# Optimization experiments

Hardware: AMD Instinct MI355X
Metric: run time of the kernel (lower is better)

The kernel has to match this reference:

```python
import jax, jax.numpy as jnp
import numpy as np

# constants from init param dict
WEIGHT = 1.0
SIGMA = 0.15          # color bandwidth
SIGMA_XY = 1.0        # spatial bandwidth
SUB_EPS = 0.01        # subtract_eps
NEG_CLASS = 0         # negative_class
NUM_CLASSES = 2
SHIFTS = ((0, 1), (1, 0), (1, 1), (1, -1))


def _shift(x, dy, dx):
    # out[..., h, w] = x[..., h+dy, w+dx]; out-of-range handled via valid mask
    return jnp.roll(x, (-dy, -dx), axis=(-2, -1))


def _valid(H, W, dy, dx, dtype):
    hs = jnp.arange(H)
    ws = jnp.arange(W)
    vh = (hs + dy >= 0) & (hs + dy < H)
    vw = (ws + dx >= 0) & (ws + dx < W)
    return (vh[:, None] & vw[None, :]).astype(dtype)  # [H, W]


def setup_inputs() -> dict:
    key = jax.random.key(0)
    k1, k2, k3 = jax.random.split(key, 3)
    B, C, H, W = 16, NUM_CLASSES, 512, 512
    # soft predictions (probabilities over classes)
    y_pr = jax.nn.softmax(jax.random.normal(k1, (B, C, H, W), dtype=jnp.float32), axis=1)
    y_gt = jnp.zeros((B, H, W), dtype=jnp.int32)  # unused by the loss
    image = jax.random.uniform(k2, (B, 3, H, W), dtype=jnp.float32)
    image_class = jax.random.randint(k3, (B,), 0, 2)
    return {"y_pr": y_pr, "y_gt": y_gt, "image": image, "image_class": image_class}


def reference(y_pr, y_gt, image, image_class):
    B, _, H, W = image.shape
    # semi-supervised selection: only images not labeled as the negative class
    sel = (image_class != NEG_CLASS).astype(y_pr.dtype)  # [B]
    loss = jnp.asarray(0.0, dtype=y_pr.dtype)
    for (dy, dx) in SHIFTS:
        v = _valid(H, W, dy, dx, y_pr.dtype)                       # [H, W]
        img_sh = _shift(image, dy, dx)                             # [B, 3, H, W]
        d2 = jnp.sum((image - img_sh) ** 2, axis=1)                # [B, H, W]
        w_xy = np.exp(-(dy * dy + dx * dx) / (2.0 * SIGMA_XY ** 2))
        mask = (jnp.exp(-d2 / (2.0 * SIGMA ** 2)) * w_xy - SUB_EPS) * v
        for ch in range(1, NUM_CLASSES):
            y = y_pr[:, ch]                                        # [B, H, W]
            pair = (y - _shift(y, dy, dx)) ** 2 * v                # [B, H, W]
            per_img = jnp.sum(mask * pair, axis=(1, 2)) / (H * W)  # [B]
            loss = loss + jnp.sum(sel * per_img) / B
    return WEIGHT * loss / len(SHIFTS)
```

## Files before the change

### kernel.cpp

```cpp
#include <hip/hip_runtime.h>


#define BATCH 16
#define HGT 512
#define WID 512
#define HW (HGT * WID)
#define SEG 8
#define SEGS_PER_ROW (WID / SEG)
#define SEGS_PER_BATCH (HGT * SEGS_PER_ROW)
#define NSEG (BATCH * SEGS_PER_BATCH)
#define NBLOCK (NSEG / 256)

__global__ __launch_bounds__(256) void crf_map(
        const float* __restrict__ y_pr,
        const float* __restrict__ image,
        const int* __restrict__ image_class,
        double* __restrict__ partial) {
    const float inv2s2 = 22.2222222f;
    const float wxy1 = 0.60653066f;
    const float wxy2 = 0.36787944f;

    const int b = blockIdx.x >> 7;
    double local = 0.0;

    if (image_class[b] != 0) {
        const int idx = blockIdx.x * 256 + threadIdx.x;
        const int seg = idx & (SEGS_PER_BATCH - 1);
        const int h = seg >> 6;
        const int w0 = (seg & 63) * SEG;
        const int hw = h * WID + w0;
        const bool hn = (h + 1 < HGT);
        const bool left = (w0 > 0);
        const bool right = (w0 + SEG < WID);

        const float* __restrict__ yb = y_pr + (size_t)b * 2 * HW + HW;
        const float* __restrict__ ib = image + (size_t)b * 3 * HW;

        float d2r[8], d2d[8], d2dr[8], d2dl[8];
        #pragma unroll
        for (int j = 0; j < 8; j++) { d2r[j] = 0.f; d2d[j] = 0.f; d2dr[j] = 0.f; d2dl[j] = 0.f; }

        #pragma unroll
        for (int c = 0; c < 3; c++) {
            const float* __restrict__ p = ib + c * HW + hw;
            float cur[9], nxt[10];
            {
                float4 a0 = *(const float4*)(p);
                float4 a1 = *(const float4*)(p + 4);
                cur[0] = a0.x; cur[1] = a0.y; cur[2] = a0.z; cur[3] = a0.w;
                cur[4] = a1.x; cur[5] = a1.y; cur[6] = a1.z; cur[7] = a1.w;
                cur[8] = right ? p[8] : 0.f;
            }
            if (hn) {
                float4 b0 = *(const float4*)(p + WID);
                float4 b1 = *(const float4*)(p + WID + 4);
                nxt[0] = left ? p[WID - 1] : 0.f;
                nxt[1] = b0.x; nxt[2] = b0.y; nxt[3] = b0.z; nxt[4] = b0.w;
                nxt[5] = b1.x; nxt[6] = b1.y; nxt[7] = b1.z; nxt[8] = b1.w;
                nxt[9] = right ? p[WID + 8] : 0.f;
            } else {
                #pragma unroll
                for (int k = 0; k < 10; k++) nxt[k] = 0.f;
            }
            #pragma unroll
            for (int j = 0; j < 8; j++) {
                float dr  = cur[j] - cur[j + 1];  d2r[j]  += dr  * dr;
                float dd  = cur[j] - nxt[j + 1];  d2d[j]  += dd  * dd;
                float ddr = cur[j] - nxt[j + 2];  d2dr[j] += ddr * ddr;
                float ddl = cur[j] - nxt[j];      d2dl[j] += ddl * ddl;
            }
        }

        float yc[9], yn[10];
        {
            const float* __restrict__ p = yb + hw;
            float4 a0 = *(const float4*)(p);
            float4 a1 = *(const float4*)(p + 4);
            yc[0] = a0.x; yc[1] = a0.y; yc[2] = a0.z; yc[3] = a0.w;
            yc[4] = a1.x; yc[5] = a1.y; yc[6] = a1.z; yc[7] = a1.w;
            yc[8] = right ? p[8] : 0.f;
            if (hn) {
                float4 b0 = *(const float4*)(p + WID);
                float4 b1 = *(const float4*)(p + WID + 4);
                yn[0] = left ? p[WID - 1] : 0.f;
                yn[1] = b0.x; yn[2] = b0.y; yn[3] = b0.z; yn[4] = b0.w;
                yn[5] = b1.x; yn[6] = b1.y; yn[7] = b1.z; yn[8] = b1.w;
                yn[9] = right ? p[WID + 8] : 0.f;
            } else {
                #pragma unroll
                for (int k = 0; k < 10; k++) yn[k] = 0.f;
            }
        }

        float s = 0.f;
        #pragma unroll
        for (int j = 0; j < 8; j++) {
            if (j < 7 || right) {
                float dy = yc[j] - yc[j + 1];
                float m = expf(-d2r[j] * inv2s2) * wxy1 - 0.01f;
                s += m * dy * dy;
            }
            if (hn) {
                {
                    float dy = yc[j] - yn[j + 1];
                    float m = expf(-d2d[j] * inv2s2) * wxy1 - 0.01f;
                    s += m * dy * dy;
                }
                if (j < 7 || right) {
                    float dy = yc[j] - yn[j + 2];
                    float m = expf(-d2dr[j] * inv2s2) * wxy2 - 0.01f;
                    s += m * dy * dy;
                }
                if (j > 0 || left) {
                    float dy = yc[j] - yn[j];
                    float m = expf(-d2dl[j] * inv2s2) * wxy2 - 0.01f;
                    s += m * dy * dy;
                }
            }
        }
        local = (double)s;
    }

    for (int off = 32; off > 0; off >>= 1)
        local += __shfl_down(local, off);

    __shared__ double sdata[4];
    const int lane = threadIdx.x & 63;
    const int wv = threadIdx.x >> 6;
    if (lane == 0) sdata[wv] = local;
    __syncthreads();
    if (threadIdx.x == 0)
        partial[blockIdx.x] = sdata[0] + sdata[1] + sdata[2] + sdata[3];
}

__global__ __launch_bounds__(256) void crf_reduce(
        const double* __restrict__ partial, float* __restrict__ out) {
    double s = 0.0;
    for (int i = threadIdx.x; i < NBLOCK; i += 256)
        s += partial[i];
    for (int off = 32; off > 0; off >>= 1)
        s += __shfl_down(s, off);
    __shared__ double sdata[4];
    const int lane = threadIdx.x & 63;
    const int wv = threadIdx.x >> 6;
    if (lane == 0) sdata[wv] = s;
    __syncthreads();
    if (threadIdx.x == 0) {
        double t = sdata[0] + sdata[1] + sdata[2] + sdata[3];
        out[0] = (float)(t * (1.0 / ((double)HW * BATCH * 4)));
    }
}

extern "C" void kernel_launch(void* const* d_in, const int* in_sizes, int n_in,
                              void* d_out, int out_size, void* d_ws, size_t ws_size,
                              hipStream_t stream) {
    const float* y_pr = (const float*)d_in[0];
    const float* image = (const float*)d_in[2];
    const int* image_class = (const int*)d_in[3];
    float* out = (float*)d_out;
    double* partial = (double*)d_ws;

    crf_map<<<NBLOCK, 256, 0, stream>>>(y_pr, image, image_class, partial);
    crf_reduce<<<1, 256, 0, stream>>>(partial, out);
}
```

Baseline: 117.3 us.

## Process two rows per thread to reuse middle row loads, use fast exp

Each thread now handles an 8-pixel segment in two consecutive rows, so the middle row's image and prediction values serve both as the lower neighbour of the first row and as the current row of the second. This cuts redundant global and cache loads from roughly two rows per output row to about one and a half, and halves the grid to 1024 blocks. It also switches expf to __expf for cheaper exponentials. The cost is higher register pressure from doubled accumulators and possibly lower occupancy.

```diff
diff --git a/kernel.cpp b/kernel.cpp
--- a/kernel.cpp
+++ b/kernel.cpp
@@ -6,10 +6,7 @@
 #define WID 512
 #define HW (HGT * WID)
 #define SEG 8
-#define SEGS_PER_ROW (WID / SEG)
-#define SEGS_PER_BATCH (HGT * SEGS_PER_ROW)
-#define NSEG (BATCH * SEGS_PER_BATCH)
-#define NBLOCK (NSEG / 256)
+#define NBLOCK 1024
 
 __global__ __launch_bounds__(256) void crf_map(
         const float* __restrict__ y_pr,
@@ -20,72 +17,98 @@
     const float wxy1 = 0.60653066f;
     const float wxy2 = 0.36787944f;
 
-    const int b = blockIdx.x >> 7;
+    const int b = blockIdx.x >> 6;
     double local = 0.0;
 
     if (image_class[b] != 0) {
-        const int idx = blockIdx.x * 256 + threadIdx.x;
-        const int seg = idx & (SEGS_PER_BATCH - 1);
-        const int h = seg >> 6;
-        const int w0 = (seg & 63) * SEG;
+        const int tid = blockIdx.x * 256 + threadIdx.x;
+        const int q = tid & 16383;
+        const int rp = q >> 6;
+        const int w0 = (q & 63) * SEG;
+        const int h = rp * 2;
         const int hw = h * WID + w0;
-        const bool hn = (h + 1 < HGT);
         const bool left = (w0 > 0);
         const bool right = (w0 + SEG < WID);
+        const bool hnB = (rp < 255);
 
         const float* __restrict__ yb = y_pr + (size_t)b * 2 * HW + HW;
         const float* __restrict__ ib = image + (size_t)b * 3 * HW;
 
-        float d2r[8], d2d[8], d2dr[8], d2dl[8];
+        float Ar[8], Ad[8], Adr[8], Adl[8];
+        float Br[8], Bd[8], Bdr[8], Bdl[8];
         #pragma unroll
-        for (int j = 0; j < 8; j++) { d2r[j] = 0.f; d2d[j] = 0.f; d2dr[j] = 0.f; d2dl[j] = 0.f; }
+        for (int j = 0; j < 8; j++) {
+            Ar[j]=0.f; Ad[j]=0.f; Adr[j]=0.f; Adl[j]=0.f;
+            Br[j]=0.f; Bd[j]=0.f; Bdr[j]=0.f; Bdl[j]=0.f;
+        }
 
         #pragma unroll
         for (int c = 0; c < 3; c++) {
             const float* __restrict__ p = ib + c * HW + hw;
-            float cur[9], nxt[10];
+            float a[9];
+            float m[10];
+            float n[10];
             {
                 float4 a0 = *(const float4*)(p);
                 float4 a1 = *(const float4*)(p + 4);
-                cur[0] = a0.x; cur[1] = a0.y; cur[2] = a0.z; cur[3] = a0.w;
-                cur[4] = a1.x; cur[5] = a1.y; cur[6] = a1.z; cur[7] = a1.w;
-                cur[8] = right ? p[8] : 0.f;
-            }
-            if (hn) {
+                a[0]=a0.x; a[1]=a0.y; a[2]=a0.z; a[3]=a0.w;
+                a[4]=a1.x; a[5]=a1.y; a[6]=a1.z; a[7]=a1.w;
+                a[8] = right ? p[8] : 0.f;
+            }
+            {
                 float4 b0 = *(const float4*)(p + WID);
                 float4 b1 = *(const float4*)(p + WID + 4);
-                nxt[0] = left ? p[WID - 1] : 0.f;
-                nxt[1] = b0.x; nxt[2] = b0.y; nxt[3] = b0.z; nxt[4] = b0.w;
-                nxt[5] = b1.x; nxt[6] = b1.y; nxt[7] = b1.z; nxt[8] = b1.w;
-                nxt[9] = right ? p[WID + 8] : 0.f;
+                m[0] = left ? p[WID - 1] : 0.f;
+                m[1]=b0.x; m[2]=b0.y; m[3]=b0.z; m[4]=b0.w;
+                m[5]=b1.x; m[6]=b1.y; m[7]=b1.z; m[8]=b1.w;
+                m[9] = right ? p[WID + 8] : 0.f;
+            }
+            if (hnB) {
+                float4 c0 = *(const float4*)(p + 2 * WID);
+                float4 c1 = *(const float4*)(p + 2 * WID + 4);
+                n[0] = left ? p[2 * WID - 1] : 0.f;
+                n[1]=c0.x; n[2]=c0.y; n[3]=c0.z; n[4]=c0.w;
+                n[5]=c1.x; n[6]=c1.y; n[7]=c1.z; n[8]=c1.w;
+                n[9] = right ? p[2 * WID + 8] : 0.f;
             } else {
                 #pragma unroll
-                for (int k = 0; k < 10; k++) nxt[k] = 0.f;
+                for (int k = 0; k < 10; k++) n[k] = 0.f;
             }
             #pragma unroll
             for (int j = 0; j < 8; j++) {
-                float dr  = cur[j] - cur[j + 1];  d2r[j]  += dr  * dr;
-                float dd  = cur[j] - nxt[j + 1];  d2d[j]  += dd  * dd;
-                float ddr = cur[j] - nxt[j + 2];  d2dr[j] += ddr * ddr;
-                float ddl = cur[j] - nxt[j];      d2dl[j] += ddl * ddl;
-            }
-        }
-
-        float yc[9], yn[10];
+                float t;
+                t = a[j] - a[j + 1];      Ar[j]  += t * t;
+                t = a[j] - m[j + 1];      Ad[j]  += t * t;
+                t = a[j] - m[j + 2];      Adr[j] += t * t;
+                t = a[j] - m[j];          Adl[j] += t * t;
+                t = m[j + 1] - m[j + 2];  Br[j]  += t * t;
+                t = m[j + 1] - n[j + 1];  Bd[j]  += t * t;
+                t = m[j + 1] - n[j + 2];  Bdr[j] += t * t;
+                t = m[j + 1] - n[j];      Bdl[j] += t * t;
+            }
+        }
+
+        float ya[9], ym[10], yn[10];
         {
             const float* __restrict__ p = yb + hw;
             float4 a0 = *(const float4*)(p);
             float4 a1 = *(const float4*)(p + 4);
-            yc[0] = a0.x; yc[1] = a0.y; yc[2] = a0.z; yc[3] = a0.w;
-            yc[4] = a1.x; yc[5] = a1.y; yc[6] = a1.z; yc[7] = a1.w;
-            yc[8] = right ? p[8] : 0.f;
-            if (hn) {
-                float4 b0 = *(const float4*)(p + WID);
-                float4 b1 = *(const float4*)(p + WID + 4);
-                yn[0] = left ? p[WID - 1] : 0.f;
-                yn[1] = b0.x; yn[2] = b0.y; yn[3] = b0.z; yn[4] = b0.w;
-                yn[5] = b1.x; yn[6] = b1.y; yn[7] = b1.z; yn[8] = b1.w;
-                yn[9] = right ? p[WID + 8] : 0.f;
+            ya[0]=a0.x; ya[1]=a0.y; ya[2]=a0.z; ya[3]=a0.w;
+            ya[4]=a1.x; ya[5]=a1.y; ya[6]=a1.z; ya[7]=a1.w;
+            ya[8] = right ? p[8] : 0.f;
+            float4 b0 = *(const float4*)(p + WID);
+            float4 b1 = *(const float4*)(p + WID + 4);
+            ym[0] = left ? p[WID - 1] : 0.f;
+            ym[1]=b0.x; ym[2]=b0.y; ym[3]=b0.z; ym[4]=b0.w;
+            ym[5]=b1.x; ym[6]=b1.y; ym[7]=b1.z; ym[8]=b1.w;
+            ym[9] = right ? p[WID + 8] : 0.f;
+            if (hnB) {
+                float4 c0 = *(const float4*)(p + 2 * WID);
+                float4 c1 = *(const float4*)(p + 2 * WID + 4);
+                yn[0] = left ? p[2 * WID - 1] : 0.f;
+                yn[1]=c0.x; yn[2]=c0.y; yn[3]=c0.z; yn[4]=c0.w;
+                yn[5]=c1.x; yn[6]=c1.y; yn[7]=c1.z; yn[8]=c1.w;
+                yn[9] = right ? p[2 * WID + 8] : 0.f;
             } else {
                 #pragma unroll
                 for (int k = 0; k < 10; k++) yn[k] = 0.f;
@@ -95,26 +118,41 @@
         float s = 0.f;
         #pragma unroll
         for (int j = 0; j < 8; j++) {
-            if (j < 7 || right) {
-                float dy = yc[j] - yc[j + 1];
-                float m = expf(-d2r[j] * inv2s2) * wxy1 - 0.01f;
-                s += m * dy * dy;
-            }
-            if (hn) {
+            const bool rj = (j < 7) || right;
+            const bool lj = (j > 0) || left;
+            float dy;
+            if (rj) {
+                dy = ya[j] - ya[j + 1];
+                s += (__expf(-Ar[j] * inv2s2) * wxy1 - 0.01f) * dy * dy;
+            }
+            {
+                dy = ya[j] - ym[j + 1];
+                s += (__expf(-Ad[j] * inv2s2) * wxy1 - 0.01f) * dy * dy;
+            }
+            if (rj) {
+                dy = ya[j] - ym[j + 2];
+                s += (__expf(-Adr[j] * inv2s2) * wxy2 - 0.01f) * dy * dy;
+            }
+            if (lj) {
+                dy = ya[j] - ym[j];
+                s += (__expf(-Adl[j] * inv2s2) * wxy2 - 0.01f) * dy * dy;
+            }
+            if (rj) {
+                dy = ym[j + 1] - ym[j + 2];
+                s += (__expf(-Br[j] * inv2s2) * wxy1 - 0.01f) * dy * dy;
+            }
+            if (hnB) {
                 {
-                    float dy = yc[j] - yn[j + 1];
-                    float m = expf(-d2d[j] * inv2s2) * wxy1 - 0.01f;
-                    s += m * dy * dy;
+                    dy = ym[j + 1] - yn[j + 1];
+                    s += (__expf(-Bd[j] * inv2s2) * wxy1 - 0.01f) * dy * dy;
                 }
-                if (j < 7 || right) {
-                    float dy = yc[j] - yn[j + 2];
-                    float m = expf(-d2dr[j] * inv2s2) * wxy2 - 0.01f;
-                    s += m * dy * dy;
+                if (rj) {
+                    dy = ym[j + 1] - yn[j + 2];
+                    s += (__expf(-Bdr[j] * inv2s2) * wxy2 - 0.01f) * dy * dy;
                 }
-                if (j > 0 || left) {
-                    float dy = yc[j] - yn[j];
-                    float m = expf(-d2dl[j] * inv2s2) * wxy2 - 0.01f;
-                    s += m * dy * dy;
+                if (lj) {
+                    dy = ym[j + 1] - yn[j];
+                    s += (__expf(-Bdl[j] * inv2s2) * wxy2 - 0.01f) * dy * dy;
                 }
             }
         }
```

Measured after the change: 113.8 us. 3.0% less time.
